# Kernel tuning notes

Hardware: AMD Instinct MI355X
Metric: run time of the kernel (lower is better)

The kernel has to match this reference:

```python
import jax, jax.numpy as jnp
import numpy as np

B, L, C, H, W = 2, 3, 64, 32, 32
DI, N, DT_RANK, K = 128, 16, 4, 4  # d_inner=2*C, d_state, dt_rank=ceil(C/16), 4 scan dirs


def setup_inputs() -> dict:
    key = jax.random.key(0)
    ks = iter(jax.random.split(key, 48))
    nrm = lambda shape, s=0.02: jax.random.normal(next(ks), shape, jnp.float32) * s
    return {
        "image_sequence": jax.random.normal(next(ks), (B, L, C, H, W), jnp.float32),
        "difficult_zone": jax.random.normal(next(ks), (B, C, H, W), jnp.float32),
        "sigma": jax.random.uniform(next(ks), (B, C, H, W), jnp.float32),
        # LayerNorm2d applied to each frame
        "norm_g": jnp.ones((C,)), "norm_b": jnp.zeros((C,)),
        # ConvolutionalResBlock (in=3C -> out=C), GroupNorm(num_groups=1)
        "gn1_g": jnp.ones((3 * C,)), "gn1_b": jnp.zeros((3 * C,)),
        "conv1_w": nrm((C, 3 * C, 3, 3)), "conv1_b": jnp.zeros((C,)),
        "gn2_g": jnp.ones((C,)), "gn2_b": jnp.zeros((C,)),
        "conv2_w": nrm((C, C, 3, 3)), "conv2_b": jnp.zeros((C,)),
        "skip_w": nrm((C, 3 * C, 1, 1)), "skip_b": jnp.zeros((C,)),
        # VSSBlock pre-norms
        "ln1_g": jnp.ones((C,)), "ln1_b": jnp.zeros((C,)),
        "ln2_g": jnp.ones((C,)), "ln2_b": jnp.zeros((C,)),
        # SS2D
        "in_proj_w": nrm((2 * DI, C)),
        "dwconv_w": nrm((DI, 1, 3, 3)), "dwconv_b": jnp.zeros((DI,)),
        "x_proj_w": nrm((K, DT_RANK + 2 * N, DI)),
        "dt_proj_w": nrm((K, DI, DT_RANK), 0.1),
        "dt_proj_b": jnp.log(jnp.expm1(jnp.full((K, DI), 0.01, jnp.float32))),
        "A_logs": jnp.log(jnp.tile(jnp.arange(1, N + 1, dtype=jnp.float32), (K * DI, 1))),
        "Ds": jnp.ones((K * DI,)),
        "out_norm_g": jnp.ones((DI,)), "out_norm_b": jnp.zeros((DI,)),
        "out_proj_w": nrm((C, DI)),
        # Mlp (hidden = C)
        "fc1_w": nrm((C, C)), "fc1_b": jnp.zeros((C,)),
        "fc2_w": nrm((C, C)), "fc2_b": jnp.zeros((C,)),
    }


def _ln(x, g, b, eps=1e-5):  # layernorm over last axis
    m = x.mean(-1, keepdims=True)
    v = x.var(-1, keepdims=True)
    return (x - m) * jax.lax.rsqrt(v + eps) * g + b


def _ln2d(x, g, b, eps=1e-6):  # per-pixel channel layernorm, NCHW
    m = x.mean(1, keepdims=True)
    v = x.var(1, keepdims=True)
    return (x - m) * jax.lax.rsqrt(v + eps) * g[None, :, None, None] + b[None, :, None, None]


def _gn1(x, g, b, eps=1e-5):  # GroupNorm(num_groups=1), NCHW
    m = x.mean((1, 2, 3), keepdims=True)
    v = x.var((1, 2, 3), keepdims=True)
    return (x - m) * jax.lax.rsqrt(v + eps) * g[None, :, None, None] + b[None, :, None, None]


def _conv(x, w, b, pad):
    y = jax.lax.conv_general_dilated(x, w, (1, 1), [(pad, pad), (pad, pad)],
                                     dimension_numbers=("NCHW", "OIHW", "NCHW"))
    return y + b[None, :, None, None]


def _forward(image_sequence, difficult_zone, sigma, norm_g, norm_b, gn1_g, gn1_b,
             conv1_w, conv1_b, gn2_g, gn2_b, conv2_w, conv2_b, skip_w, skip_b,
             ln1_g, ln1_b, ln2_g, ln2_b, in_proj_w, dwconv_w, dwconv_b, x_proj_w,
             dt_proj_w, dt_proj_b, A_logs, Ds, out_norm_g, out_norm_b, out_proj_w,
             fc1_w, fc1_b, fc2_w, fc2_b):
    b, l, c, h, w = image_sequence.shape
    bl, L2 = b * l, h * w
    # fold frame loop into batch (identical math per frame in the torch loop)
    frames = _ln2d(image_sequence.reshape(bl, c, h, w), norm_g, norm_b)
    dz = jnp.broadcast_to(difficult_zone[:, None], (b, l, c, h, w)).reshape(bl, c, h, w)
    sg = jnp.broadcast_to(sigma[:, None], (b, l, c, h, w)).reshape(bl, c, h, w)
    x = jnp.concatenate([dz, frames, sg], axis=1)  # [bl, 3c, h, w]
    # channel compressor: pre-act conv res block
    hdn = _conv(jax.nn.silu(_gn1(x, gn1_g, gn1_b)), conv1_w, conv1_b, 1)
    hdn = _conv(jax.nn.silu(_gn1(hdn, gn2_g, gn2_b)), conv2_w, conv2_b, 1)
    x = hdn + _conv(x, skip_w, skip_b, 0)          # [bl, c, h, w]
    x = x.transpose(0, 2, 3, 1)                    # [bl, h, w, c]
    # --- VSSBlock (pre-norm): x = x + SS2D(LN(x)) ---
    xn = _ln(x, ln1_g, ln1_b)
    xz = xn @ in_proj_w.T                          # [bl,h,w,2*DI]
    xc, z = jnp.split(xz, 2, axis=-1)
    xc = xc.transpose(0, 3, 1, 2)                  # [bl, DI, h, w]
    xc = jax.lax.conv_general_dilated(xc, dwconv_w, (1, 1), [(1, 1), (1, 1)],
                                      dimension_numbers=("NCHW", "OIHW", "NCHW"),
                                      feature_group_count=DI) + dwconv_b[None, :, None, None]
    xc = jax.nn.silu(xc)
    # 4-direction scan inputs (HW, WH, and their reverses)
    xf = xc.reshape(bl, DI, L2)
    xt = xc.transpose(0, 1, 3, 2).reshape(bl, DI, L2)
    xs = jnp.stack([xf, xt], axis=1)
    xs = jnp.concatenate([xs, jnp.flip(xs, axis=-1)], axis=1)  # [bl, 4, DI, L2]
    x_dbl = jnp.einsum("bkdl,kcd->bkcl", xs, x_proj_w)
    dts, Bs, Cs = jnp.split(x_dbl, [DT_RANK, DT_RANK + N], axis=2)
    dts = jnp.einsum("bkrl,kdr->bkdl", dts, dt_proj_w) + dt_proj_b[None, :, :, None]
    dts = jax.nn.softplus(dts)                     # [bl, 4, DI, L2]
    A = -jnp.exp(A_logs).reshape(K, DI, N)
    dA = jnp.exp(dts[..., None] * A[None, :, :, None, :])            # [bl,4,DI,L2,N]
    dBu = dts[..., None] * Bs.transpose(0, 1, 3, 2)[:, :, None] * xs[..., None]
    a_t = dA.transpose(3, 0, 1, 2, 4)              # [L2, bl, 4, DI, N]
    bu_t = dBu.transpose(3, 0, 1, 2, 4)
    c_t = Cs.transpose(3, 0, 1, 2)                 # [L2, bl, 4, N]

    def step(hid, inp):
        a_i, bu_i, c_i = inp
        hid = a_i * hid + bu_i
        return hid, jnp.einsum("bkdn,bkn->bkd", hid, c_i)

    h0 = jnp.zeros((bl, K, DI, N), xs.dtype)
    _, ys = jax.lax.scan(step, h0, (a_t, bu_t, c_t))                 # [L2, bl, 4, DI]
    ys = ys.transpose(1, 2, 3, 0) + xs * Ds.reshape(K, DI)[None, :, :, None]
    inv = jnp.flip(ys[:, 2:4], axis=-1)
    y = (ys[:, 0] + inv[:, 0]
         + ys[:, 1].reshape(bl, DI, w, h).transpose(0, 1, 3, 2).reshape(bl, DI, L2)
         + inv[:, 1].reshape(bl, DI, w, h).transpose(0, 1, 3, 2).reshape(bl, DI, L2))
    y = _ln(y.transpose(0, 2, 1), out_norm_g, out_norm_b).reshape(bl, h, w, DI)
    y = y * jax.nn.silu(z)
    x = x + y @ out_proj_w.T
    # --- x = x + Mlp(LN(x)) ---
    xn = _ln(x, ln2_g, ln2_b)
    x = x + (jax.nn.gelu(xn @ fc1_w.T + fc1_b, approximate=False) @ fc2_w.T + fc2_b)
    return x.transpose(0, 3, 1, 2).reshape(b, l, c, h, w)


def reference(image_sequence, difficult_zone, sigma, norm_g, norm_b, gn1_g, gn1_b,
              conv1_w, conv1_b, gn2_g, gn2_b, conv2_w, conv2_b, skip_w, skip_b,
              ln1_g, ln1_b, ln2_g, ln2_b, in_proj_w, dwconv_w, dwconv_b, x_proj_w,
              dt_proj_w, dt_proj_b, A_logs, Ds, out_norm_g, out_norm_b, out_proj_w,
              fc1_w, fc1_b, fc2_w, fc2_b):
    return _forward(image_sequence, difficult_zone, sigma, norm_g, norm_b, gn1_g, gn1_b,
                    conv1_w, conv1_b, gn2_g, gn2_b, conv2_w, conv2_b, skip_w, skip_b,
                    ln1_g, ln1_b, ln2_g, ln2_b, in_proj_w, dwconv_w, dwconv_b, x_proj_w,
                    dt_proj_w, dt_proj_b, A_logs, Ds, out_norm_g, out_norm_b, out_proj_w,
                    fc1_w, fc1_b, fc2_w, fc2_b)
```

## Files before the change

### kernel.cpp

```cpp
#include <hip/hip_runtime.h>
#include <math.h>

#define BL    6
#define CCH   64
#define C3    192
#define L2    1024
#define DIC   128
#define NST   16
#define K4    4
#define PSTR  1088
#define NCH   32

#define LOG2E 1.44269504088896340736f
#define LN2C  0.69314718055994530942f

__device__ __forceinline__ float fexp(float x){ return __builtin_amdgcn_exp2f(x*LOG2E); }
__device__ __forceinline__ float fsilu(float x){ return x / (1.f + fexp(-x)); }
__device__ __forceinline__ float fsoftplus(float x){
  if (x > 20.f) return x;
  return __builtin_amdgcn_logf(1.f + fexp(x)) * LN2C;
}
__device__ __forceinline__ float fgelu(float x){
  return 0.5f*x*(1.f + erff(x*0.70710678118654752440f));
}

__global__ __launch_bounds__(256) void k_ln2d(const float* __restrict__ img,
    const float* __restrict__ dz, const float* __restrict__ sg,
    const float* __restrict__ g, const float* __restrict__ b, float* __restrict__ x3c,
    float* __restrict__ psum1, float* __restrict__ psq1){
  __shared__ float ps[4][16], pq[4][16], gs[4], gq[4];
  int s = blockIdx.x >> 6;
  int pg = blockIdx.x & 63;
  int tid = threadIdx.x;
  int px = tid & 15; int cg = tid >> 4;
  int wv = tid >> 6; int lane = tid & 63;
  int p = pg*16 + px;
  int bsmp = s/3;
  const float* fr = img + (size_t)s*CCH*L2;
  float vals[4]; float sm=0.f, sq=0.f;
  #pragma unroll
  for (int j=0;j<4;++j){
    int c = cg*4 + j;
    float v = fr[c*L2 + p];
    vals[j]=v; sm+=v; sq+=v*v;
  }
  sm += __shfl_xor(sm,16,64); sq += __shfl_xor(sq,16,64);
  sm += __shfl_xor(sm,32,64); sq += __shfl_xor(sq,32,64);
  if (lane < 16){ ps[wv][lane]=sm; pq[wv][lane]=sq; }
  __syncthreads();
  sm = ps[0][px]+ps[1][px]+ps[2][px]+ps[3][px];
  sq = pq[0][px]+pq[1][px]+pq[2][px]+pq[3][px];
  float mean = sm*(1.f/CCH); float var = sq*(1.f/CCH)-mean*mean;
  float rs = rsqrtf(var + 1e-6f);
  float* o = x3c + (size_t)s*C3*L2;
  const float* dzp = dz + (size_t)bsmp*CCH*L2;
  const float* sgp = sg + (size_t)bsmp*CCH*L2;
  float gsm=0.f, gsq=0.f;
  #pragma unroll
  for (int j=0;j<4;++j){
    int c = cg*4+j;
    float dzv = dzp[c*L2+p];
    float nv  = (vals[j]-mean)*rs*g[c] + b[c];
    float sgv = sgp[c*L2+p];
    o[c*L2+p] = dzv;
    o[(CCH+c)*L2+p] = nv;
    o[(2*CCH+c)*L2+p] = sgv;
    gsm += dzv+nv+sgv; gsq += dzv*dzv+nv*nv+sgv*sgv;
  }
  for (int m=1;m<64;m<<=1){ gsm+=__shfl_xor(gsm,m,64); gsq+=__shfl_xor(gsq,m,64); }
  if (lane==0){ gs[wv]=gsm; gq[wv]=gsq; }
  __syncthreads();
  if (tid==0){
    psum1[blockIdx.x] = gs[0]+gs[1]+gs[2]+gs[3];
    psq1 [blockIdx.x] = gq[0]+gq[1]+gq[2]+gq[3];
  }
}

__global__ __launch_bounds__(256) void k_gnact_pad(const float* __restrict__ x,
    const float* __restrict__ psum, const float* __restrict__ psq,
    const float* __restrict__ g, const float* __restrict__ b,
    int ch, int parts, float inv_n, float eps, float* __restrict__ out){
  int bx = blockIdx.x;
  int s = bx / ch; int c = bx % ch;
  int tid = threadIdx.x;
  float sm=0.f, sq=0.f;
  for (int i=0;i<parts;++i){ sm += psum[s*parts+i]; sq += psq[s*parts+i]; }
  float mean = sm*inv_n;
  float var = sq*inv_n - mean*mean;
  float rs = rsqrtf(var + eps);
  float gc = g[c]*rs; float bc = b[c] - mean*rs*g[c];
  float4 v = *(const float4*)(x + (size_t)bx*1024 + tid*4);
  float4 o; o.x = fsilu(v.x*gc+bc); o.y = fsilu(v.y*gc+bc);
  o.z = fsilu(v.z*gc+bc); o.w = fsilu(v.w*gc+bc);
  float* pl = out + (size_t)bx*PSTR;
  *(float4*)(pl + 32 + tid*4) = o;
  float4 z4 = make_float4(0.f,0.f,0.f,0.f);
  if (tid < 8)  *(float4*)(pl + tid*4) = z4;
  else if (tid < 16) *(float4*)(pl + 1056 + (tid-8)*4) = z4;
}

__device__ __forceinline__ void conv_row_acc(float4& a0, float4& a1, float4 mid, float lf, float rt,
    const float* wp0, const float* wp1){
  float w0=wp0[0], w1=wp0[1], w2=wp0[2];
  a0.x = fmaf(w0,lf,   fmaf(w1,mid.x, fmaf(w2,mid.y, a0.x)));
  a0.y = fmaf(w0,mid.x,fmaf(w1,mid.y, fmaf(w2,mid.z, a0.y)));
  a0.z = fmaf(w0,mid.y,fmaf(w1,mid.z, fmaf(w2,mid.w, a0.z)));
  a0.w = fmaf(w0,mid.z,fmaf(w1,mid.w, fmaf(w2,rt,    a0.w)));
  float v0=wp1[0], v1=wp1[1], v2=wp1[2];
  a1.x = fmaf(v0,lf,   fmaf(v1,mid.x, fmaf(v2,mid.y, a1.x)));
  a1.y = fmaf(v0,mid.x,fmaf(v1,mid.y, fmaf(v2,mid.z, a1.y)));
  a1.z = fmaf(v0,mid.y,fmaf(v1,mid.z, fmaf(v2,mid.w, a1.z)));
  a1.w = fmaf(v0,mid.z,fmaf(v1,mid.w, fmaf(v2,rt,    a1.w)));
}

__device__ __forceinline__ void conv_ci_body(float4 m0, float4 m1, float4 m2, int q,
    const float* wp0, const float* wp1, float4& a0, float4& a1){
  float lf0=__shfl_up(m0.w,1,64), rt0=__shfl_down(m0.x,1,64);
  float lf1=__shfl_up(m1.w,1,64), rt1=__shfl_down(m1.x,1,64);
  float lf2=__shfl_up(m2.w,1,64), rt2=__shfl_down(m2.x,1,64);
  if (q==0){ lf0=0.f; lf1=0.f; lf2=0.f; }
  if (q==7){ rt0=0.f; rt1=0.f; rt2=0.f; }
  conv_row_acc(a0,a1,m0,lf0,rt0, wp0+0, wp1+0);
  conv_row_acc(a0,a1,m1,lf1,rt1, wp0+3, wp1+3);
  conv_row_acc(a0,a1,m2,lf2,rt2, wp0+6, wp1+6);
}

__global__ __launch_bounds__(256) void k_conv1_split(const float* __restrict__ xact,
    const float* __restrict__ w, float* __restrict__ part){
  int bx = blockIdx.x; int kk = bx&7; int cop=(bx>>3)&31; int s=bx>>8;
  int co0 = cop*2, co1 = co0+1;
  int tid = threadIdx.x; int row = tid>>3; int q = tid&7; int col0 = q*4;
  float4 a0 = make_float4(0.f,0.f,0.f,0.f);
  float4 a1 = make_float4(0.f,0.f,0.f,0.f);
  int ci0 = kk*24;
  const float* pl = xact + ((size_t)s*C3 + ci0)*PSTR + row*32 + col0;
  const float* wp0 = w + (size_t)(co0*C3 + ci0)*9;
  const float* wp1 = w + (size_t)(co1*C3 + ci0)*9;
  float4 m0 = *(const float4*)(pl);
  float4 m1 = *(const float4*)(pl+32);
  float4 m2 = *(const float4*)(pl+64);
  #pragma unroll 2
  for (int i=0;i<24;++i){
    const float* pn = pl + (i<23 ? PSTR : 0);
    float4 n0 = *(const float4*)(pn);
    float4 n1 = *(const float4*)(pn+32);
    float4 n2 = *(const float4*)(pn+64);
    conv_ci_body(m0,m1,m2,q, wp0, wp1, a0, a1);
    wp0 += 9; wp1 += 9; pl = pn; m0=n0; m1=n1; m2=n2;
  }
  float* pp = part + (size_t)kk*(BL*CCH*L2) + ((size_t)s*CCH+co0)*L2 + row*32+col0;
  *(float4*)pp = a0;
  *(float4*)(pp+L2) = a1;
}

__global__ __launch_bounds__(256) void k_reduce1(const float* __restrict__ part,
    const float* __restrict__ bias, float* __restrict__ h1,
    float* __restrict__ psum2, float* __restrict__ psq2){
  int co = blockIdx.x & 63; int s = blockIdx.x >> 6;
  size_t ofs = ((size_t)s*CCH+co)*L2 + threadIdx.x*4;
  const size_t stride = (size_t)BL*CCH*L2;
  float4 acc = *(const float4*)(part + ofs);
  #pragma unroll
  for (int kk=1;kk<8;++kk){
    float4 r = *(const float4*)(part + (size_t)kk*stride + ofs);
    acc.x += r.x; acc.y += r.y; acc.z += r.z; acc.w += r.w;
  }
  float bv = bias[co];
  acc.x += bv; acc.y += bv; acc.z += bv; acc.w += bv;
  *(float4*)(h1 + ofs) = acc;
  float sm = acc.x+acc.y+acc.z+acc.w;
  float sq = acc.x*acc.x+acc.y*acc.y+acc.z*acc.z+acc.w*acc.w;
  for (int m=1;m<64;m<<=1){ sm+=__shfl_xor(sm,m,64); sq+=__shfl_xor(sq,m,64); }
  __shared__ float s_sm[4], s_sq[4];
  int wv = threadIdx.x>>6;
  if ((threadIdx.x&63)==0){ s_sm[wv]=sm; s_sq[wv]=sq; }
  __syncthreads();
  if (threadIdx.x==0){
    psum2[blockIdx.x] = s_sm[0]+s_sm[1]+s_sm[2]+s_sm[3];
    psq2 [blockIdx.x] = s_sq[0]+s_sq[1]+s_sq[2]+s_sq[3];
  }
}

__global__ __launch_bounds__(256) void k_conv2_split(const float* __restrict__ xact2,
    const float* __restrict__ x3c, const float* __restrict__ w2,
    const float* __restrict__ wsk, float* __restrict__ part){
  int t = blockIdx.x; int role = t % 3; t /= 3;
  int cop = t & 31; int s = t >> 5;
  int co0 = cop*2, co1 = co0+1;
  int tid = threadIdx.x; int row = tid>>3; int q = tid&7; int col0 = q*4;
  int p = row*32+col0;
  float4 a0 = make_float4(0.f,0.f,0.f,0.f);
  float4 a1 = make_float4(0.f,0.f,0.f,0.f);
  if (role < 2){
    int ci0 = role*32;
    const float* pl = xact2 + ((size_t)s*CCH + ci0)*PSTR + row*32 + col0;
    const float* wp0 = w2 + (size_t)(co0*CCH + ci0)*9;
    const float* wp1 = w2 + (size_t)(co1*CCH + ci0)*9;
    float4 m0 = *(const float4*)(pl);
    float4 m1 = *(const float4*)(pl+32);
    float4 m2 = *(const float4*)(pl+64);
    #pragma unroll 2
    for (int i=0;i<32;++i){
      const float* pn = pl + (i<31 ? PSTR : 0);
      float4 n0 = *(const float4*)(pn);
      float4 n1 = *(const float4*)(pn+32);
      float4 n2 = *(const float4*)(pn+64);
      conv_ci_body(m0,m1,m2,q, wp0, wp1, a0, a1);
      wp0 += 9; wp1 += 9; pl = pn; m0=n0; m1=n1; m2=n2;
    }
  } else {
    const float* x3 = x3c + (size_t)s*C3*L2 + p;
    #pragma unroll 4
    for (int ci=0; ci<C3; ++ci){
      float4 v = *(const float4*)(x3 + (size_t)ci*L2);
      float ws0 = wsk[co0*C3+ci], ws1 = wsk[co1*C3+ci];
      a0.x = fmaf(ws0,v.x,a0.x); a0.y = fmaf(ws0,v.y,a0.y); a0.z = fmaf(ws0,v.z,a0.z); a0.w = fmaf(ws0,v.w,a0.w);
      a1.x = fmaf(ws1,v.x,a1.x); a1.y = fmaf(ws1,v.y,a1.y); a1.z = fmaf(ws1,v.z,a1.z); a1.w = fmaf(ws1,v.w,a1.w);
    }
  }
  float* pp = part + (size_t)role*(BL*CCH*L2) + ((size_t)s*CCH+co0)*L2 + p;
  *(float4*)pp = a0;
  *(float4*)(pp+L2) = a1;
}

__global__ __launch_bounds__(256) void k_reduce2(const float* __restrict__ part,
    const float* __restrict__ b2, const float* __restrict__ bsk,
    float* __restrict__ xp, float* __restrict__ x_cmaj){
  int co = blockIdx.x & 63; int s = blockIdx.x >> 6;
  int p = threadIdx.x*4;
  size_t ofs = ((size_t)s*CCH+co)*L2 + p;
  const size_t stride = (size_t)BL*CCH*L2;
  float4 r0 = *(const float4*)(part + ofs);
  float4 r1 = *(const float4*)(part + stride + ofs);
  float4 r2 = *(const float4*)(part + 2*stride + ofs);
  float bv = b2[co]+bsk[co];
  float4 o;
  o.x = r0.x+r1.x+r2.x+bv;
  o.y = r0.y+r1.y+r2.y+bv;
  o.z = r0.z+r1.z+r2.z+bv;
  o.w = r0.w+r1.w+r2.w+bv;
  *(float4*)(x_cmaj + ofs) = o;
  float* xpb = xp + ((size_t)s*L2 + p)*CCH + co;
  xpb[0] = o.x; xpb[CCH] = o.y; xpb[2*CCH] = o.z; xpb[3*CCH] = o.w;
}

__global__ __launch_bounds__(256) void k_ln1_inproj(const float* __restrict__ xp,
    const float* __restrict__ g, const float* __restrict__ b, const float* __restrict__ W,
    float* __restrict__ xc, float* __restrict__ z_t){
  __shared__ float xn_s[64*65];
  int bx = blockIdx.x; int oq = bx & 3; int pg = (bx>>2)&15; int s = bx>>6;
  int p0 = pg*64;
  int tid = threadIdx.x; int wv = __builtin_amdgcn_readfirstlane(tid>>6); int lane = tid&63;
  for (int j=0;j<16;++j){
    int pl = wv*16 + j; int p = p0 + pl;
    float v = xp[((size_t)s*L2 + p)*CCH + lane];
    float sm = v, sq = v*v;
    for (int m=1;m<64;m<<=1){ sm += __shfl_xor(sm,m,64); sq += __shfl_xor(sq,m,64); }
    float mean = sm*(1.f/64.f); float var = sq*(1.f/64.f) - mean*mean;
    float rs = rsqrtf(var + 1e-5f);
    xn_s[pl*65 + lane] = (v-mean)*rs*g[lane] + b[lane];
  }
  __syncthreads();
  int px_l = tid & 63;
  int og = __builtin_amdgcn_readfirstlane(tid >> 6);
  int o0 = oq*64 + og*16;
  float acc[16];
  #pragma unroll
  for (int oi=0;oi<16;++oi) acc[oi]=0.f;
  for (int c=0;c<64;++c){
    float xv = xn_s[px_l*65 + c];
    #pragma unroll
    for (int oi=0;oi<16;++oi) acc[oi] = fmaf(W[(o0+oi)*64 + c], xv, acc[oi]);
  }
  int p = p0 + px_l;
  if (oq < 2){
    #pragma unroll
    for (int oi=0;oi<16;++oi) xc[((size_t)s*DIC + o0 + oi)*L2 + p] = acc[oi];
  } else {
    #pragma unroll
    for (int oi=0;oi<16;++oi) z_t[((size_t)s*DIC + (o0-128) + oi)*L2 + p] = acc[oi];
  }
}

__global__ __launch_bounds__(256) void k_dwconv(const float* __restrict__ xc,
    const float* __restrict__ w, const float* __restrict__ bias, float* __restrict__ xconv){
  int bx = blockIdx.x; int dch = bx & 127; int s = bx >> 7;
  int tid = threadIdx.x; int row = tid>>3; int q = tid&7; int col0 = q*4;
  const float* xr = xc + ((size_t)s*DIC+dch)*L2;
  const float* wp = w + dch*9;
  float bv = bias[dch];
  float4 acc = make_float4(bv,bv,bv,bv);
  #pragma unroll
  for (int dy=-1;dy<=1;++dy){
    int r = row+dy;
    float4 mid = make_float4(0.f,0.f,0.f,0.f);
    if (0<=r && r<32) mid = *(const float4*)(xr + r*32 + col0);
    float lf = __shfl_up(mid.w,1,64); if(q==0) lf=0.f;
    float rt = __shfl_down(mid.x,1,64); if(q==7) rt=0.f;
    float w0=wp[(dy+1)*3], w1=wp[(dy+1)*3+1], w2=wp[(dy+1)*3+2];
    acc.x = fmaf(w0,lf,   fmaf(w1,mid.x, fmaf(w2,mid.y, acc.x)));
    acc.y = fmaf(w0,mid.x,fmaf(w1,mid.y, fmaf(w2,mid.z, acc.y)));
    acc.z = fmaf(w0,mid.y,fmaf(w1,mid.z, fmaf(w2,mid.w, acc.z)));
    acc.w = fmaf(w0,mid.z,fmaf(w1,mid.w, fmaf(w2,rt,    acc.w)));
  }
  acc.x = fsilu(acc.x); acc.y = fsilu(acc.y); acc.z = fsilu(acc.z); acc.w = fsilu(acc.w);
  *(float4*)(xconv + ((size_t)s*DIC+dch)*L2 + row*32+col0) = acc;
}

__global__ __launch_bounds__(256) void k_xproj_dt(const float* __restrict__ xconv,
    const float* __restrict__ W,
    float* __restrict__ dtr, float* __restrict__ Bp, float* __restrict__ Cp,
    float* __restrict__ u_t){
  __shared__ float smem[128*68];
  int bx = blockIdx.x; int pg = bx & 15; int sk = bx >> 4;
  int k = sk & 3; int s = sk >> 2;
  int tid = threadIdx.x;
  for (int i = tid; i < 128*16; i += 256){
    int dr = i>>4; int j4 = (i&15)*4;
    float4 v = *(const float4*)(xconv + ((size_t)(s*DIC + dr))*L2 + pg*64 + j4);
    *(float4*)&smem[dr*68 + j4] = v;
  }
  __syncthreads();
  if (k == 0){
    float* ub = u_t + ((size_t)(s*L2) + pg*64)*DIC;
    for (int i = tid; i < 64*128; i += 256){
      int px2 = i>>7; int dd = i&127;
      ub[(size_t)px2*DIC + dd] = smem[dd*68 + px2];
    }
  }
  int px = tid & 63;
  int cgrp = __builtin_amdgcn_readfirstlane(tid >> 6);
  int c0 = cgrp*9;
  const float* wb = W + (size_t)(k*36 + c0)*DIC;
  float acc[9];
  #pragma unroll
  for (int ci=0;ci<9;++ci) acc[ci]=0.f;
  for (int d=0; d<DIC; ++d){
    float xv = smem[d*68 + px];
    #pragma unroll
    for (int ci=0;ci<9;++ci) acc[ci] = fmaf(wb[ci*DIC+d], xv, acc[ci]);
  }
  __syncthreads();
  #pragma unroll
  for (int ci=0;ci<9;++ci) smem[(c0+ci)*68 + px] = acc[ci];
  __syncthreads();
  {
    int pp = tid >> 2; int r = tid & 3;
    dtr[((size_t)sk*L2 + pg*64 + pp)*4 + r] = smem[r*68 + pp];
  }
  float* Bb = Bp + ((size_t)sk*L2 + pg*64)*NST;
  float* Cb = Cp + ((size_t)sk*L2 + pg*64)*NST;
  for (int i = tid; i < 1024; i += 256){
    int pp = i>>4; int n = i&15;
    Bb[pp*NST + n] = smem[(4+n)*68 + pp];
    Cb[pp*NST + n] = smem[(20+n)*68 + pp];
  }
}

__device__ __forceinline__ int scan_pix32(int ch, int j, int k){
  if (k==0) return ch*32 + j;
  if (k==1) return j*32 + ch;
  if (k==2) return 1023 - (ch*32 + j);
  return 1023 - (j*32 + ch);
}

struct StepB { float4 dt4; float uv; float4 B0,B1,B2,B3; };
__device__ __forceinline__ StepB loadB(const float* dr, const float* ub, const float* Bb, int p){
  StepB r;
  r.dt4 = *(const float4*)(dr + (size_t)p*4);
  r.uv = ub[(size_t)p*DIC];
  const float* bp = Bb + p*NST;
  r.B0 = *(const float4*)bp; r.B1 = *(const float4*)(bp+4);
  r.B2 = *(const float4*)(bp+8); r.B3 = *(const float4*)(bp+12);
  return r;
}
__device__ __forceinline__ float dt_eval(float4 w4, float bb, float4 d4){
  return fsoftplus(fmaf(w4.x,d4.x,fmaf(w4.y,d4.y,fmaf(w4.z,d4.z,fmaf(w4.w,d4.w,bb)))));
}

__global__ __launch_bounds__(256,2) void k_scan_part3(const float* __restrict__ dtr,
    const float* __restrict__ dtw, const float* __restrict__ dtb,
    const float* __restrict__ u_t, const float* __restrict__ Bp,
    const float* __restrict__ A_logs, float* __restrict__ hend, float* __restrict__ Ssum){
  int bx = blockIdx.x; int chp = bx & 15; int sk = bx >> 4;
  int k = sk & 3; int s = sk >> 2;
  int tid = threadIdx.x; int d = tid & 127; int ch = chp*2 + (tid>>7);
  float aco[16];
  {
    const float* ab = A_logs + (size_t)(k*DIC+d)*NST;
    #pragma unroll
    for (int n=0;n<16;++n) aco[n] = -LOG2E * fexp(ab[n]);
  }
  float4 w4 = *(const float4*)(dtw + (size_t)(k*DIC+d)*4);
  float bb = dtb[k*DIC+d];
  float h[16]; float Sacc = 0.f;
  #pragma unroll
  for (int n=0;n<16;++n) h[n]=0.f;
  const float* dr = dtr + (size_t)sk*L2*4;
  const float* ub = u_t + (size_t)s*L2*DIC + d;
  const float* Bb = Bp + (size_t)sk*L2*NST;
  StepB cur = loadB(dr, ub, Bb, scan_pix32(ch, 0, k));
  #pragma unroll 4
  for (int j=0;j<32;++j){
// ... 143 lines not shown
    int p = pg*16 + px;
    size_t base = ((size_t)s*CCH + c0)*L2 + p;
    xvt[(c0+0)*17 + px] = x_cmaj[base]      + a0;
    xvt[(c0+1)*17 + px] = x_cmaj[base+L2]   + a1;
    xvt[(c0+2)*17 + px] = x_cmaj[base+2*L2] + a2;
    xvt[(c0+3)*17 + px] = x_cmaj[base+3*L2] + a3;
  }
  __syncthreads();
  int px = tid & 15; int cgp = tid >> 4;
  float sm=0.f, sq=0.f;
  for (int c=0;c<64;++c){ float v = xvt[c*17+px]; sm+=v; sq+=v*v; }
  float mean = sm*(1.f/64.f);
  float rs = rsqrtf(sq*(1.f/64.f) - mean*mean + 1e-5f);
  int o0 = cgp*4;
  float t[4];
  #pragma unroll
  for (int oi=0;oi<4;++oi) t[oi] = b1[o0+oi];
  for (int c=0;c<64;++c){
    float xn = (xvt[c*17+px]-mean)*rs*g2[c] + b2n[c];
    #pragma unroll
    for (int oi=0;oi<4;++oi) t[oi] = fmaf(xn, w1[(o0+oi)*64 + c], t[oi]);
  }
  #pragma unroll
  for (int oi=0;oi<4;++oi) ts[(o0+oi)*17 + px] = fgelu(t[oi]);
  __syncthreads();
  int c0 = cgp*4;
  float acc[4];
  #pragma unroll
  for (int ci=0;ci<4;++ci) acc[ci] = xvt[(c0+ci)*17+px] + b2[c0+ci];
  for (int o=0;o<64;++o){
    float tv = ts[o*17+px];
    #pragma unroll
    for (int ci=0;ci<4;++ci) acc[ci] = fmaf(tv, w2[(c0+ci)*64 + o], acc[ci]);
  }
  int p = pg*16 + px;
  #pragma unroll
  for (int ci=0;ci<4;++ci) out[((size_t)s*CCH + c0+ci)*L2 + p] = acc[ci];
}

extern "C" void kernel_launch(void* const* d_in, const int* in_sizes, int n_in,
                              void* d_out, int out_size, void* d_ws, size_t ws_size,
                              hipStream_t stream){
  (void)in_sizes; (void)n_in; (void)out_size; (void)ws_size;
  const float* img      = (const float*)d_in[0];
  const float* dz       = (const float*)d_in[1];
  const float* sg       = (const float*)d_in[2];
  const float* norm_g   = (const float*)d_in[3];
  const float* norm_b   = (const float*)d_in[4];
  const float* gn1_g    = (const float*)d_in[5];
  const float* gn1_b    = (const float*)d_in[6];
  const float* conv1_w  = (const float*)d_in[7];
  const float* conv1_b  = (const float*)d_in[8];
  const float* gn2_g    = (const float*)d_in[9];
  const float* gn2_b    = (const float*)d_in[10];
  const float* conv2_w  = (const float*)d_in[11];
  const float* conv2_b  = (const float*)d_in[12];
  const float* skip_w   = (const float*)d_in[13];
  const float* skip_b   = (const float*)d_in[14];
  const float* ln1_g    = (const float*)d_in[15];
  const float* ln1_b    = (const float*)d_in[16];
  const float* ln2_g    = (const float*)d_in[17];
  const float* ln2_b    = (const float*)d_in[18];
  const float* in_proj_w= (const float*)d_in[19];
  const float* dwconv_w = (const float*)d_in[20];
  const float* dwconv_b = (const float*)d_in[21];
  const float* x_proj_w = (const float*)d_in[22];
  const float* dt_proj_w= (const float*)d_in[23];
  const float* dt_proj_b= (const float*)d_in[24];
  const float* A_logs   = (const float*)d_in[25];
  const float* Ds       = (const float*)d_in[26];
  const float* out_norm_g = (const float*)d_in[27];
  const float* out_norm_b = (const float*)d_in[28];
  const float* out_proj_w = (const float*)d_in[29];
  const float* fc1_w    = (const float*)d_in[30];
  const float* fc1_b    = (const float*)d_in[31];
  const float* fc2_w    = (const float*)d_in[32];
  const float* fc2_b    = (const float*)d_in[33];

  float* ws = (float*)d_ws;
  float* x3c    = ws;
  float* xact1  = x3c    + 1179648;
  float* h1     = xact1  + 1253376;
  float* xact2  = h1     + 393216;
  float* xp     = xact2  + 417792;
  float* x_cmaj = xp     + 393216;
  float* z_t    = x_cmaj + 393216;
  float* xc     = z_t    + 786432;
  float* xconv  = xc     + 786432;
  float* hole   = xconv  + 786432;
  float* scanbuf= hole   + 884736;
  float* ys_t   = scanbuf+ 3145728;
  float* statsb = ys_t   + 3145728;
  float* psum1  = statsb;
  float* psq1   = statsb + 384;
  float* psum2  = statsb + 768;
  float* psq2   = statsb + 1152;
  float* part1  = scanbuf;
  float* part2  = ys_t;
  float* hend   = x3c;
  float* u_t    = h1;
  float* Bp     = xp;
  float* Cp     = xc;
  float* dtr    = hole;
  float* Ssum   = hole + 98304;
  float* Hin    = scanbuf;

  k_ln2d<<<384, 256, 0, stream>>>(img, dz, sg, norm_g, norm_b, x3c, psum1, psq1);
  k_gnact_pad<<<6*C3, 256, 0, stream>>>(x3c, psum1, psq1, gn1_g, gn1_b, C3, 64,
                                        1.f/(C3*L2), 1e-5f, xact1);
  k_conv1_split<<<1536, 256, 0, stream>>>(xact1, conv1_w, part1);
  k_reduce1<<<384, 256, 0, stream>>>(part1, conv1_b, h1, psum2, psq2);
  k_gnact_pad<<<6*CCH, 256, 0, stream>>>(h1, psum2, psq2, gn2_g, gn2_b, CCH, 64,
                                         1.f/(CCH*L2), 1e-5f, xact2);
  k_conv2_split<<<576, 256, 0, stream>>>(xact2, x3c, conv2_w, skip_w, part2);
  k_reduce2<<<384, 256, 0, stream>>>(part2, conv2_b, skip_b, xp, x_cmaj);
  k_ln1_inproj<<<384, 256, 0, stream>>>(xp, ln1_g, ln1_b, in_proj_w, xc, z_t);
  k_dwconv<<<768, 256, 0, stream>>>(xc, dwconv_w, dwconv_b, xconv);
  k_xproj_dt<<<384, 256, 0, stream>>>(xconv, x_proj_w, dtr, Bp, Cp, u_t);
  k_scan_part3<<<384, 256, 0, stream>>>(dtr, dt_proj_w, dt_proj_b, u_t, Bp, A_logs, hend, Ssum);
  k_scan_fix3<<<192, 256, 0, stream>>>(hend, Ssum, A_logs, Hin);
  k_scan_y3<<<384, 256, 0, stream>>>(dtr, dt_proj_w, dt_proj_b, u_t, Bp, Cp, A_logs, Ds, Hin, ys_t);
  k_tail<<<384, 256, 0, stream>>>(ys_t, z_t, out_norm_g, out_norm_b, out_proj_w, x_cmaj,
                                  ln2_g, ln2_b, fc1_w, fc1_b, fc2_w, fc2_b, (float*)d_out);
}
```

Baseline: 304.7 us.

## Fuse GroupNorm+SiLU into convs, reduce2 into LN1/in_proj, dwconv into x_proj

New measurement: 372.0 us. +22.1%, slower.

```diff
diff --git a/kernel.cpp b/kernel.cpp
--- a/kernel.cpp
+++ b/kernel.cpp
@@ -8,7 +8,6 @@
 #define DIC   128
 #define NST   16
 #define K4    4
-#define PSTR  1088
 #define NCH   32
 
 #define LOG2E 1.44269504088896340736f
@@ -76,29 +75,6 @@
   }
 }
 
-__global__ __launch_bounds__(256) void k_gnact_pad(const float* __restrict__ x,
-    const float* __restrict__ psum, const float* __restrict__ psq,
-    const float* __restrict__ g, const float* __restrict__ b,
-    int ch, int parts, float inv_n, float eps, float* __restrict__ out){
-  int bx = blockIdx.x;
-  int s = bx / ch; int c = bx % ch;
-  int tid = threadIdx.x;
-  float sm=0.f, sq=0.f;
-  for (int i=0;i<parts;++i){ sm += psum[s*parts+i]; sq += psq[s*parts+i]; }
-  float mean = sm*inv_n;
-  float var = sq*inv_n - mean*mean;
-  float rs = rsqrtf(var + eps);
-  float gc = g[c]*rs; float bc = b[c] - mean*rs*g[c];
-  float4 v = *(const float4*)(x + (size_t)bx*1024 + tid*4);
-  float4 o; o.x = fsilu(v.x*gc+bc); o.y = fsilu(v.y*gc+bc);
-  o.z = fsilu(v.z*gc+bc); o.w = fsilu(v.w*gc+bc);
-  float* pl = out + (size_t)bx*PSTR;
-  *(float4*)(pl + 32 + tid*4) = o;
-  float4 z4 = make_float4(0.f,0.f,0.f,0.f);
-  if (tid < 8)  *(float4*)(pl + tid*4) = z4;
-  else if (tid < 16) *(float4*)(pl + 1056 + (tid-8)*4) = z4;
-}
-
 __device__ __forceinline__ void conv_row_acc(float4& a0, float4& a1, float4 mid, float lf, float rt,
     const float* wp0, const float* wp1){
   float w0=wp0[0], w1=wp0[1], w2=wp0[2];
@@ -125,28 +101,49 @@
   conv_row_acc(a0,a1,m2,lf2,rt2, wp0+6, wp1+6);
 }
 
-__global__ __launch_bounds__(256) void k_conv1_split(const float* __restrict__ xact,
+__device__ __forceinline__ float4 act4(float4 v, float gc, float bc){
+  float4 o;
+  o.x = fsilu(v.x*gc+bc); o.y = fsilu(v.y*gc+bc);
+  o.z = fsilu(v.z*gc+bc); o.w = fsilu(v.w*gc+bc);
+  return o;
+}
+
+__global__ __launch_bounds__(256) void k_conv1_act(const float* __restrict__ x3c,
+    const float* __restrict__ psum, const float* __restrict__ psq,
+    const float* __restrict__ g, const float* __restrict__ b,
     const float* __restrict__ w, float* __restrict__ part){
   int bx = blockIdx.x; int kk = bx&7; int cop=(bx>>3)&31; int s=bx>>8;
   int co0 = cop*2, co1 = co0+1;
   int tid = threadIdx.x; int row = tid>>3; int q = tid&7; int col0 = q*4;
-  float4 a0 = make_float4(0.f,0.f,0.f,0.f);
-  float4 a1 = make_float4(0.f,0.f,0.f,0.f);
+  float sm=0.f, sq_=0.f;
+  for (int i=0;i<64;++i){ sm += psum[s*64+i]; sq_ += psq[s*64+i]; }
+  float mean = sm*(1.f/(C3*L2));
+  float var = sq_*(1.f/(C3*L2)) - mean*mean;
+  float rs = rsqrtf(var + 1e-5f);
+  float4 z4 = make_float4(0.f,0.f,0.f,0.f);
+  float4 a0 = z4, a1 = z4;
   int ci0 = kk*24;
-  const float* pl = xact + ((size_t)s*C3 + ci0)*PSTR + row*32 + col0;
+  bool v0 = (row > 0), v2 = (row < 31);
+  const float* plane = x3c + ((size_t)s*C3 + ci0)*L2 + col0;
   const float* wp0 = w + (size_t)(co0*C3 + ci0)*9;
   const float* wp1 = w + (size_t)(co1*C3 + ci0)*9;
-  float4 m0 = *(const float4*)(pl);
-  float4 m1 = *(const float4*)(pl+32);
-  float4 m2 = *(const float4*)(pl+64);
+  float4 r0 = v0 ? *(const float4*)(plane + (row-1)*32) : z4;
+  float4 r1 =      *(const float4*)(plane + row*32);
+  float4 r2 = v2 ? *(const float4*)(plane + (row+1)*32) : z4;
   #pragma unroll 2
   for (int i=0;i<24;++i){
-    const float* pn = pl + (i<23 ? PSTR : 0);
-    float4 n0 = *(const float4*)(pn);
-    float4 n1 = *(const float4*)(pn+32);
-    float4 n2 = *(const float4*)(pn+64);
+    const float* pn = plane + (i<23 ? L2 : 0);
+    float4 n0 = v0 ? *(const float4*)(pn + (row-1)*32) : z4;
+    float4 n1 =      *(const float4*)(pn + row*32);
+    float4 n2 = v2 ? *(const float4*)(pn + (row+1)*32) : z4;
+    int c = ci0 + i;
+    float gw = g[c];
+    float gc = gw*rs; float bc = b[c] - mean*rs*gw;
+    float4 m0 = v0 ? act4(r0,gc,bc) : z4;
+    float4 m1 = act4(r1,gc,bc);
+    float4 m2 = v2 ? act4(r2,gc,bc) : z4;
     conv_ci_body(m0,m1,m2,q, wp0, wp1, a0, a1);
-    wp0 += 9; wp1 += 9; pl = pn; m0=n0; m1=n1; m2=n2;
+    wp0 += 9; wp1 += 9; plane = pn; r0=n0; r1=n1; r2=n2;
   }
   float* pp = part + (size_t)kk*(BL*CCH*L2) + ((size_t)s*CCH+co0)*L2 + row*32+col0;
   *(float4*)pp = a0;
@@ -181,32 +178,47 @@
   }
 }
 
-__global__ __launch_bounds__(256) void k_conv2_split(const float* __restrict__ xact2,
-    const float* __restrict__ x3c, const float* __restrict__ w2,
-    const float* __restrict__ wsk, float* __restrict__ part){
+__global__ __launch_bounds__(256) void k_conv2_act(const float* __restrict__ h1,
+    const float* __restrict__ x3c,
+    const float* __restrict__ psum, const float* __restrict__ psq,
+    const float* __restrict__ g, const float* __restrict__ b,
+    const float* __restrict__ w2, const float* __restrict__ wsk,
+    float* __restrict__ part){
   int t = blockIdx.x; int role = t % 3; t /= 3;
   int cop = t & 31; int s = t >> 5;
   int co0 = cop*2, co1 = co0+1;
   int tid = threadIdx.x; int row = tid>>3; int q = tid&7; int col0 = q*4;
   int p = row*32+col0;
-  float4 a0 = make_float4(0.f,0.f,0.f,0.f);
-  float4 a1 = make_float4(0.f,0.f,0.f,0.f);
+  float4 z4 = make_float4(0.f,0.f,0.f,0.f);
+  float4 a0 = z4, a1 = z4;
   if (role < 2){
+    float sm=0.f, sq_=0.f;
+    for (int i=0;i<64;++i){ sm += psum[s*64+i]; sq_ += psq[s*64+i]; }
+    float mean = sm*(1.f/(CCH*L2));
+    float var = sq_*(1.f/(CCH*L2)) - mean*mean;
+    float rs = rsqrtf(var + 1e-5f);
     int ci0 = role*32;
-    const float* pl = xact2 + ((size_t)s*CCH + ci0)*PSTR + row*32 + col0;
+    bool v0 = (row > 0), v2 = (row < 31);
+    const float* plane = h1 + ((size_t)s*CCH + ci0)*L2 + col0;
     const float* wp0 = w2 + (size_t)(co0*CCH + ci0)*9;
     const float* wp1 = w2 + (size_t)(co1*CCH + ci0)*9;
-    float4 m0 = *(const float4*)(pl);
-    float4 m1 = *(const float4*)(pl+32);
-    float4 m2 = *(const float4*)(pl+64);
+    float4 r0 = v0 ? *(const float4*)(plane + (row-1)*32) : z4;
+    float4 r1 =      *(const float4*)(plane + row*32);
+    float4 r2 = v2 ? *(const float4*)(plane + (row+1)*32) : z4;
     #pragma unroll 2
     for (int i=0;i<32;++i){
-      const float* pn = pl + (i<31 ? PSTR : 0);
-      float4 n0 = *(const float4*)(pn);
-      float4 n1 = *(const float4*)(pn+32);
-      float4 n2 = *(const float4*)(pn+64);
+      const float* pn = plane + (i<31 ? L2 : 0);
+      float4 n0 = v0 ? *(const float4*)(pn + (row-1)*32) : z4;
+      float4 n1 =      *(const float4*)(pn + row*32);
+      float4 n2 = v2 ? *(const float4*)(pn + (row+1)*32) : z4;
+      int c = ci0 + i;
+      float gw = g[c];
+      float gc = gw*rs; float bc = b[c] - mean*rs*gw;
+      float4 m0 = v0 ? act4(r0,gc,bc) : z4;
+      float4 m1 = act4(r1,gc,bc);
+      float4 m2 = v2 ? act4(r2,gc,bc) : z4;
       conv_ci_body(m0,m1,m2,q, wp0, wp1, a0, a1);
-      wp0 += 9; wp1 += 9; pl = pn; m0=n0; m1=n1; m2=n2;
+      wp0 += 9; wp1 += 9; plane = pn; r0=n0; r1=n1; r2=n2;
     }
   } else {
     const float* x3 = x3c + (size_t)s*C3*L2 + p;
@@ -223,42 +235,48 @@
   *(float4*)(pp+L2) = a1;
 }
 
-__global__ __launch_bounds__(256) void k_reduce2(const float* __restrict__ part,
+__global__ __launch_bounds__(256) void k_red2_ln1_inproj(const float* __restrict__ part,
     const float* __restrict__ b2, const float* __restrict__ bsk,
-    float* __restrict__ xp, float* __restrict__ x_cmaj){
-  int co = blockIdx.x & 63; int s = blockIdx.x >> 6;
-  int p = threadIdx.x*4;
-  size_t ofs = ((size_t)s*CCH+co)*L2 + p;
-  const size_t stride = (size_t)BL*CCH*L2;
-  float4 r0 = *(const float4*)(part + ofs);
-  float4 r1 = *(const float4*)(part + stride + ofs);
-  float4 r2 = *(const float4*)(part + 2*stride + ofs);
-  float bv = b2[co]+bsk[co];
-  float4 o;
-  o.x = r0.x+r1.x+r2.x+bv;
-  o.y = r0.y+r1.y+r2.y+bv;
-  o.z = r0.z+r1.z+r2.z+bv;
-  o.w = r0.w+r1.w+r2.w+bv;
-  *(float4*)(x_cmaj + ofs) = o;
-  float* xpb = xp + ((size_t)s*L2 + p)*CCH + co;
-  xpb[0] = o.x; xpb[CCH] = o.y; xpb[2*CCH] = o.z; xpb[3*CCH] = o.w;
-}
-
-__global__ __launch_bounds__(256) void k_ln1_inproj(const float* __restrict__ xp,
-    const float* __restrict__ g, const float* __restrict__ b, const float* __restrict__ W,
-    float* __restrict__ xc, float* __restrict__ z_t){
+    const float* __restrict__ g, const float* __restrict__ b,
+    const float* __restrict__ W,
+    float* __restrict__ x_cmaj, float* __restrict__ xc, float* __restrict__ z_t){
   __shared__ float xn_s[64*65];
   int bx = blockIdx.x; int oq = bx & 3; int pg = (bx>>2)&15; int s = bx>>6;
   int p0 = pg*64;
-  int tid = threadIdx.x; int wv = __builtin_amdgcn_readfirstlane(tid>>6); int lane = tid&63;
-  for (int j=0;j<16;++j){
-    int pl = wv*16 + j; int p = p0 + pl;
-    float v = xp[((size_t)s*L2 + p)*CCH + lane];
-    float sm = v, sq = v*v;
-    for (int m=1;m<64;m<<=1){ sm += __shfl_xor(sm,m,64); sq += __shfl_xor(sq,m,64); }
-    float mean = sm*(1.f/64.f); float var = sq*(1.f/64.f) - mean*mean;
-    float rs = rsqrtf(var + 1e-5f);
-    xn_s[pl*65 + lane] = (v-mean)*rs*g[lane] + b[lane];
+  int tid = threadIdx.x;
+  const size_t stride = (size_t)BL*CCH*L2;
+  #pragma unroll
+  for (int kq=0;kq<4;++kq){
+    int f = kq*256 + tid;
+    int co = f >> 4; int px4 = (f & 15)*4;
+    size_t ofs = ((size_t)s*CCH+co)*L2 + p0 + px4;
+    float4 r0 = *(const float4*)(part + ofs);
+    float4 r1 = *(const float4*)(part + stride + ofs);
+    float4 r2 = *(const float4*)(part + 2*stride + ofs);
+    float bv = b2[co]+bsk[co];
+    float4 o;
+    o.x = r0.x+r1.x+r2.x+bv;
+    o.y = r0.y+r1.y+r2.y+bv;
+    o.z = r0.z+r1.z+r2.z+bv;
+    o.w = r0.w+r1.w+r2.w+bv;
+    if (oq == 0) *(float4*)(x_cmaj + ofs) = o;
+    xn_s[(px4+0)*65 + co] = o.x;
+    xn_s[(px4+1)*65 + co] = o.y;
+    xn_s[(px4+2)*65 + co] = o.z;
+    xn_s[(px4+3)*65 + co] = o.w;
+  }
+  __syncthreads();
+  {
+    int wv = __builtin_amdgcn_readfirstlane(tid>>6); int lane = tid&63;
+    for (int j=0;j<16;++j){
+      int pl = wv*16 + j;
+      float v = xn_s[pl*65 + lane];
+      float sm = v, sq = v*v;
+      for (int m=1;m<64;m<<=1){ sm += __shfl_xor(sm,m,64); sq += __shfl_xor(sq,m,64); }
+      float mean = sm*(1.f/64.f); float var = sq*(1.f/64.f) - mean*mean;
+      float rs = rsqrtf(var + 1e-5f);
+      xn_s[pl*65 + lane] = (v-mean)*rs*g[lane] + b[lane];
+    }
   }
   __syncthreads();
   int px_l = tid & 63;
@@ -282,32 +300,8 @@
   }
 }
 
-__global__ __launch_bounds__(256) void k_dwconv(const float* __restrict__ xc,
-    const float* __restrict__ w, const float* __restrict__ bias, float* __restrict__ xconv){
-  int bx = blockIdx.x; int dch = bx & 127; int s = bx >> 7;
-  int tid = threadIdx.x; int row = tid>>3; int q = tid&7; int col0 = q*4;
-  const float* xr = xc + ((size_t)s*DIC+dch)*L2;
-  const float* wp = w + dch*9;
-  float bv = bias[dch];
-  float4 acc = make_float4(bv,bv,bv,bv);
-  #pragma unroll
-  for (int dy=-1;dy<=1;++dy){
-    int r = row+dy;
-    float4 mid = make_float4(0.f,0.f,0.f,0.f);
-    if (0<=r && r<32) mid = *(const float4*)(xr + r*32 + col0);
-    float lf = __shfl_up(mid.w,1,64); if(q==0) lf=0.f;
-    float rt = __shfl_down(mid.x,1,64); if(q==7) rt=0.f;
-    float w0=wp[(dy+1)*3], w1=wp[(dy+1)*3+1], w2=wp[(dy+1)*3+2];
-    acc.x = fmaf(w0,lf,   fmaf(w1,mid.x, fmaf(w2,mid.y, acc.x)));
-    acc.y = fmaf(w0,mid.x,fmaf(w1,mid.y, fmaf(w2,mid.z, acc.y)));
-    acc.z = fmaf(w0,mid.y,fmaf(w1,mid.z, fmaf(w2,mid.w, acc.z)));
-    acc.w = fmaf(w0,mid.z,fmaf(w1,mid.w, fmaf(w2,rt,    acc.w)));
-  }
-  acc.x = fsilu(acc.x); acc.y = fsilu(acc.y); acc.z = fsilu(acc.z); acc.w = fsilu(acc.w);
-  *(float4*)(xconv + ((size_t)s*DIC+dch)*L2 + row*32+col0) = acc;
-}
-
-__global__ __launch_bounds__(256) void k_xproj_dt(const float* __restrict__ xconv,
+__global__ __launch_bounds__(256) void k_xproj_dt(const float* __restrict__ xc,
+    const float* __restrict__ dww, const float* __restrict__ dwb,
     const float* __restrict__ W,
     float* __restrict__ dtr, float* __restrict__ Bp, float* __restrict__ Cp,
     float* __restrict__ u_t){
@@ -317,8 +311,28 @@
   int tid = threadIdx.x;
   for (int i = tid; i < 128*16; i += 256){
     int dr = i>>4; int j4 = (i&15)*4;
-    float4 v = *(const float4*)(xconv + ((size_t)(s*DIC + dr))*L2 + pg*64 + j4);
-    *(float4*)&smem[dr*68 + j4] = v;
+    int rw = j4>>5; int col0 = j4 & 31;
+    int gr = pg*2 + rw;
+    int q = i&7;
+    const float* xr = xc + ((size_t)s*DIC+dr)*L2;
+    const float* wp = dww + dr*9;
+    float bv = dwb[dr];
+    float4 acc = make_float4(bv,bv,bv,bv);
+    #pragma unroll
+    for (int dy=-1;dy<=1;++dy){
+      int r = gr+dy;
+      float4 mid = make_float4(0.f,0.f,0.f,0.f);
+      if (0<=r && r<32) mid = *(const float4*)(xr + r*32 + col0);
+      float lf = __shfl_up(mid.w,1,64); if(q==0) lf=0.f;
+      float rt = __shfl_down(mid.x,1,64); if(q==7) rt=0.f;
+      float w0=wp[(dy+1)*3], w1=wp[(dy+1)*3+1], w2=wp[(dy+1)*3+2];
+      acc.x = fmaf(w0,lf,   fmaf(w1,mid.x, fmaf(w2,mid.y, acc.x)));
+      acc.y = fmaf(w0,mid.x,fmaf(w1,mid.y, fmaf(w2,mid.z, acc.y)));
+      acc.z = fmaf(w0,mid.y,fmaf(w1,mid.z, fmaf(w2,mid.w, acc.z)));
+      acc.w = fmaf(w0,mid.z,fmaf(w1,mid.w, fmaf(w2,rt,    acc.w)));
+    }
+    acc.x = fsilu(acc.x); acc.y = fsilu(acc.y); acc.z = fsilu(acc.z); acc.w = fsilu(acc.w);
+    *(float4*)&smem[dr*68 + j4] = acc;
   }
   __syncthreads();
   if (k == 0){
@@ -628,8 +642,8 @@
   float* xact1  = x3c    + 1179648;
   float* h1     = xact1  + 1253376;
   float* xact2  = h1     + 393216;
-  float* xp     = xact2  + 417792;
-  float* x_cmaj = xp     + 393216;
+  float* xpslot = xact2  + 417792;
+  float* x_cmaj = xpslot + 393216;
   float* z_t    = x_cmaj + 393216;
   float* xc     = z_t    + 786432;
   float* xconv  = xc     + 786432;
@@ -645,24 +659,19 @@
   float* part2  = ys_t;
   float* hend   = x3c;
   float* u_t    = h1;
-  float* Bp     = xp;
-  float* Cp     = xc;
+  float* Bp     = xpslot;
   float* dtr    = hole;
   float* Ssum   = hole + 98304;
+  float* Cp     = hole + 196608;
   float* Hin    = scanbuf;
 
   k_ln2d<<<384, 256, 0, stream>>>(img, dz, sg, norm_g, norm_b, x3c, psum1, psq1);
-  k_gnact_pad<<<6*C3, 256, 0, stream>>>(x3c, psum1, psq1, gn1_g, gn1_b, C3, 64,
-                                        1.f/(C3*L2), 1e-5f, xact1);
-  k_conv1_split<<<1536, 256, 0, stream>>>(xact1, conv1_w, part1);
+  k_conv1_act<<<1536, 256, 0, stream>>>(x3c, psum1, psq1, gn1_g, gn1_b, conv1_w, part1);
   k_reduce1<<<384, 256, 0, stream>>>(part1, conv1_b, h1, psum2, psq2);
-  k_gnact_pad<<<6*CCH, 256, 0, stream>>>(h1, psum2, psq2, gn2_g, gn2_b, CCH, 64,
-                                         1.f/(CCH*L2), 1e-5f, xact2);
-  k_conv2_split<<<576, 256, 0, stream>>>(xact2, x3c, conv2_w, skip_w, part2);
-  k_reduce2<<<384, 256, 0, stream>>>(part2, conv2_b, skip_b, xp, x_cmaj);
-  k_ln1_inproj<<<384, 256, 0, stream>>>(xp, ln1_g, ln1_b, in_proj_w, xc, z_t);
-  k_dwconv<<<768, 256, 0, stream>>>(xc, dwconv_w, dwconv_b, xconv);
-  k_xproj_dt<<<384, 256, 0, stream>>>(xconv, x_proj_w, dtr, Bp, Cp, u_t);
+  k_conv2_act<<<576, 256, 0, stream>>>(h1, x3c, psum2, psq2, gn2_g, gn2_b, conv2_w, skip_w, part2);
+  k_red2_ln1_inproj<<<384, 256, 0, stream>>>(part2, conv2_b, skip_b, ln1_g, ln1_b, in_proj_w,
+                                             x_cmaj, xc, z_t);
+  k_xproj_dt<<<384, 256, 0, stream>>>(xc, dwconv_w, dwconv_b, x_proj_w, dtr, Bp, Cp, u_t);
   k_scan_part3<<<384, 256, 0, stream>>>(dtr, dt_proj_w, dt_proj_b, u_t, Bp, A_logs, hend, Ssum);
   k_scan_fix3<<<192, 256, 0, stream>>>(hend, Ssum, A_logs, Hin);
   k_scan_y3<<<384, 256, 0, stream>>>(dtr, dt_proj_w, dt_proj_b, u_t, Bp, Cp, A_logs, Ds, Hin, ys_t);
```

## Fuse reduce2 into LN1/in_proj and fold depthwise conv into x_proj

Applied to the files above, without the earlier changes.

Measured after the change: 305.3 us. About the same (+0.2%).

```diff
diff --git a/kernel.cpp b/kernel.cpp
--- a/kernel.cpp
+++ b/kernel.cpp
@@ -15,7 +15,7 @@
 #define LN2C  0.69314718055994530942f
 
 __device__ __forceinline__ float fexp(float x){ return __builtin_amdgcn_exp2f(x*LOG2E); }
-__device__ __forceinline__ float fsilu(float x){ return x / (1.f + fexp(-x)); }
+__device__ __forceinline__ float fsilu(float x){ return x * __builtin_amdgcn_rcpf(1.f + fexp(-x)); }
 __device__ __forceinline__ float fsoftplus(float x){
   if (x > 20.f) return x;
   return __builtin_amdgcn_logf(1.f + fexp(x)) * LN2C;
@@ -223,42 +223,48 @@
   *(float4*)(pp+L2) = a1;
 }
 
-__global__ __launch_bounds__(256) void k_reduce2(const float* __restrict__ part,
+__global__ __launch_bounds__(256) void k_red2_ln1_inproj(const float* __restrict__ part,
     const float* __restrict__ b2, const float* __restrict__ bsk,
-    float* __restrict__ xp, float* __restrict__ x_cmaj){
-  int co = blockIdx.x & 63; int s = blockIdx.x >> 6;
-  int p = threadIdx.x*4;
-  size_t ofs = ((size_t)s*CCH+co)*L2 + p;
-  const size_t stride = (size_t)BL*CCH*L2;
-  float4 r0 = *(const float4*)(part + ofs);
-  float4 r1 = *(const float4*)(part + stride + ofs);
-  float4 r2 = *(const float4*)(part + 2*stride + ofs);
-  float bv = b2[co]+bsk[co];
-  float4 o;
-  o.x = r0.x+r1.x+r2.x+bv;
-  o.y = r0.y+r1.y+r2.y+bv;
-  o.z = r0.z+r1.z+r2.z+bv;
-  o.w = r0.w+r1.w+r2.w+bv;
-  *(float4*)(x_cmaj + ofs) = o;
-  float* xpb = xp + ((size_t)s*L2 + p)*CCH + co;
-  xpb[0] = o.x; xpb[CCH] = o.y; xpb[2*CCH] = o.z; xpb[3*CCH] = o.w;
-}
-
-__global__ __launch_bounds__(256) void k_ln1_inproj(const float* __restrict__ xp,
-    const float* __restrict__ g, const float* __restrict__ b, const float* __restrict__ W,
-    float* __restrict__ xc, float* __restrict__ z_t){
+    const float* __restrict__ g, const float* __restrict__ b,
+    const float* __restrict__ W,
+    float* __restrict__ x_cmaj, float* __restrict__ xc, float* __restrict__ z_t){
   __shared__ float xn_s[64*65];
   int bx = blockIdx.x; int oq = bx & 3; int pg = (bx>>2)&15; int s = bx>>6;
   int p0 = pg*64;
-  int tid = threadIdx.x; int wv = __builtin_amdgcn_readfirstlane(tid>>6); int lane = tid&63;
-  for (int j=0;j<16;++j){
-    int pl = wv*16 + j; int p = p0 + pl;
-    float v = xp[((size_t)s*L2 + p)*CCH + lane];
-    float sm = v, sq = v*v;
-    for (int m=1;m<64;m<<=1){ sm += __shfl_xor(sm,m,64); sq += __shfl_xor(sq,m,64); }
-    float mean = sm*(1.f/64.f); float var = sq*(1.f/64.f) - mean*mean;
-    float rs = rsqrtf(var + 1e-5f);
-    xn_s[pl*65 + lane] = (v-mean)*rs*g[lane] + b[lane];
+  int tid = threadIdx.x;
+  const size_t stride = (size_t)BL*CCH*L2;
+  #pragma unroll
+  for (int kq=0;kq<4;++kq){
+    int f = kq*256 + tid;
+    int co = f >> 4; int px4 = (f & 15)*4;
+    size_t ofs = ((size_t)s*CCH+co)*L2 + p0 + px4;
+    float4 r0 = *(const float4*)(part + ofs);
+    float4 r1 = *(const float4*)(part + stride + ofs);
+    float4 r2 = *(const float4*)(part + 2*stride + ofs);
+    float bv = b2[co]+bsk[co];
+    float4 o;
+    o.x = r0.x+r1.x+r2.x+bv;
+    o.y = r0.y+r1.y+r2.y+bv;
+    o.z = r0.z+r1.z+r2.z+bv;
+    o.w = r0.w+r1.w+r2.w+bv;
+    if (oq == 0) *(float4*)(x_cmaj + ofs) = o;
+    xn_s[(px4+0)*65 + co] = o.x;
+    xn_s[(px4+1)*65 + co] = o.y;
+    xn_s[(px4+2)*65 + co] = o.z;
+    xn_s[(px4+3)*65 + co] = o.w;
+  }
+  __syncthreads();
+  {
+    int wv = __builtin_amdgcn_readfirstlane(tid>>6); int lane = tid&63;
+    for (int j=0;j<16;++j){
+      int pl = wv*16 + j;
+      float v = xn_s[pl*65 + lane];
+      float sm = v, sq = v*v;
+      for (int m=1;m<64;m<<=1){ sm += __shfl_xor(sm,m,64); sq += __shfl_xor(sq,m,64); }
+      float mean = sm*(1.f/64.f); float var = sq*(1.f/64.f) - mean*mean;
+      float rs = rsqrtf(var + 1e-5f);
+      xn_s[pl*65 + lane] = (v-mean)*rs*g[lane] + b[lane];
+    }
   }
   __syncthreads();
   int px_l = tid & 63;
@@ -282,32 +288,8 @@
   }
 }
 
-__global__ __launch_bounds__(256) void k_dwconv(const float* __restrict__ xc,
-    const float* __restrict__ w, const float* __restrict__ bias, float* __restrict__ xconv){
-  int bx = blockIdx.x; int dch = bx & 127; int s = bx >> 7;
-  int tid = threadIdx.x; int row = tid>>3; int q = tid&7; int col0 = q*4;
-  const float* xr = xc + ((size_t)s*DIC+dch)*L2;
-  const float* wp = w + dch*9;
-  float bv = bias[dch];
-  float4 acc = make_float4(bv,bv,bv,bv);
-  #pragma unroll
-  for (int dy=-1;dy<=1;++dy){
-    int r = row+dy;
-    float4 mid = make_float4(0.f,0.f,0.f,0.f);
-    if (0<=r && r<32) mid = *(const float4*)(xr + r*32 + col0);
-    float lf = __shfl_up(mid.w,1,64); if(q==0) lf=0.f;
-    float rt = __shfl_down(mid.x,1,64); if(q==7) rt=0.f;
-    float w0=wp[(dy+1)*3], w1=wp[(dy+1)*3+1], w2=wp[(dy+1)*3+2];
-    acc.x = fmaf(w0,lf,   fmaf(w1,mid.x, fmaf(w2,mid.y, acc.x)));
-    acc.y = fmaf(w0,mid.x,fmaf(w1,mid.y, fmaf(w2,mid.z, acc.y)));
-    acc.z = fmaf(w0,mid.y,fmaf(w1,mid.z, fmaf(w2,mid.w, acc.z)));
-    acc.w = fmaf(w0,mid.z,fmaf(w1,mid.w, fmaf(w2,rt,    acc.w)));
-  }
-  acc.x = fsilu(acc.x); acc.y = fsilu(acc.y); acc.z = fsilu(acc.z); acc.w = fsilu(acc.w);
-  *(float4*)(xconv + ((size_t)s*DIC+dch)*L2 + row*32+col0) = acc;
-}
-
-__global__ __launch_bounds__(256) void k_xproj_dt(const float* __restrict__ xconv,
+__global__ __launch_bounds__(256) void k_xproj_dt(const float* __restrict__ xc,
+    const float* __restrict__ dww, const float* __restrict__ dwb,
     const float* __restrict__ W,
     float* __restrict__ dtr, float* __restrict__ Bp, float* __restrict__ Cp,
     float* __restrict__ u_t){
@@ -317,8 +299,28 @@
   int tid = threadIdx.x;
   for (int i = tid; i < 128*16; i += 256){
     int dr = i>>4; int j4 = (i&15)*4;
-    float4 v = *(const float4*)(xconv + ((size_t)(s*DIC + dr))*L2 + pg*64 + j4);
-    *(float4*)&smem[dr*68 + j4] = v;
+    int rw = j4>>5; int col0 = j4 & 31;
+    int gr = pg*2 + rw;
+    int q = i&7;
+    const float* xr = xc + ((size_t)s*DIC+dr)*L2;
+    const float* wp = dww + dr*9;
+    float bv = dwb[dr];
+    float4 acc = make_float4(bv,bv,bv,bv);
+    #pragma unroll
+    for (int dy=-1;dy<=1;++dy){
+      int r = gr+dy;
+      float4 mid = make_float4(0.f,0.f,0.f,0.f);
+      if (0<=r && r<32) mid = *(const float4*)(xr + r*32 + col0);
+      float lf = __shfl_up(mid.w,1,64); if(q==0) lf=0.f;
+      float rt = __shfl_down(mid.x,1,64); if(q==7) rt=0.f;
+      float w0=wp[(dy+1)*3], w1=wp[(dy+1)*3+1], w2=wp[(dy+1)*3+2];
+      acc.x = fmaf(w0,lf,   fmaf(w1,mid.x, fmaf(w2,mid.y, acc.x)));
+      acc.y = fmaf(w0,mid.x,fmaf(w1,mid.y, fmaf(w2,mid.z, acc.y)));
+      acc.z = fmaf(w0,mid.y,fmaf(w1,mid.z, fmaf(w2,mid.w, acc.z)));
+      acc.w = fmaf(w0,mid.z,fmaf(w1,mid.w, fmaf(w2,rt,    acc.w)));
+    }
+    acc.x = fsilu(acc.x); acc.y = fsilu(acc.y); acc.z = fsilu(acc.z); acc.w = fsilu(acc.w);
+    *(float4*)&smem[dr*68 + j4] = acc;
   }
   __syncthreads();
   if (k == 0){
@@ -628,12 +630,12 @@
   float* xact1  = x3c    + 1179648;
   float* h1     = xact1  + 1253376;
   float* xact2  = h1     + 393216;
-  float* xp     = xact2  + 417792;
-  float* x_cmaj = xp     + 393216;
+  float* xpslot = xact2  + 417792;
+  float* x_cmaj = xpslot + 393216;
   float* z_t    = x_cmaj + 393216;
   float* xc     = z_t    + 786432;
-  float* xconv  = xc     + 786432;
-  float* hole   = xconv  + 786432;
+  float* cpslot = xc     + 786432;
+  float* hole   = cpslot + 786432;
   float* scanbuf= hole   + 884736;
   float* ys_t   = scanbuf+ 3145728;
   float* statsb = ys_t   + 3145728;
@@ -645,8 +647,8 @@
   float* part2  = ys_t;
   float* hend   = x3c;
   float* u_t    = h1;
-  float* Bp     = xp;
-  float* Cp     = xc;
+  float* Bp     = xpslot;
+  float* Cp     = cpslot;
   float* dtr    = hole;
   float* Ssum   = hole + 98304;
   float* Hin    = scanbuf;
@@ -659,10 +661,9 @@
   k_gnact_pad<<<6*CCH, 256, 0, stream>>>(h1, psum2, psq2, gn2_g, gn2_b, CCH, 64,
                                          1.f/(CCH*L2), 1e-5f, xact2);
   k_conv2_split<<<576, 256, 0, stream>>>(xact2, x3c, conv2_w, skip_w, part2);
-  k_reduce2<<<384, 256, 0, stream>>>(part2, conv2_b, skip_b, xp, x_cmaj);
-  k_ln1_inproj<<<384, 256, 0, stream>>>(xp, ln1_g, ln1_b, in_proj_w, xc, z_t);
-  k_dwconv<<<768, 256, 0, stream>>>(xc, dwconv_w, dwconv_b, xconv);
-  k_xproj_dt<<<384, 256, 0, stream>>>(xconv, x_proj_w, dtr, Bp, Cp, u_t);
+  k_red2_ln1_inproj<<<384, 256, 0, stream>>>(part2, conv2_b, skip_b, ln1_g, ln1_b, in_proj_w,
+                                             x_cmaj, xc, z_t);
+  k_xproj_dt<<<384, 256, 0, stream>>>(xc, dwconv_w, dwconv_b, x_proj_w, dtr, Bp, Cp, u_t);
   k_scan_part3<<<384, 256, 0, stream>>>(dtr, dt_proj_w, dt_proj_b, u_t, Bp, A_logs, hend, Ssum);
   k_scan_fix3<<<192, 256, 0, stream>>>(hend, Ssum, A_logs, Hin);
   k_scan_y3<<<384, 256, 0, stream>>>(dtr, dt_proj_w, dt_proj_b, u_t, Bp, Cp, A_logs, Ds, Hin, ys_t);
```
